# Kernel tuning notes

Measured on AMD Instinct MI355X. Metric: run time of the kernel, lower is better.

Reference implementation:

```python
import jax, jax.numpy as jnp
import numpy as np

N = 100000
E = 3200000
D = 64  # in_feats == hidden_feats == 64 (hardcoded in module)


def setup_inputs() -> dict:
    key = jax.random.key(0)
    ks = jax.random.split(key, 12)
    s = 1.0 / np.sqrt(D)
    return {
        "x": jax.random.normal(ks[0], (N, D), dtype=jnp.float32),
        "edge_index": jax.random.randint(ks[1], (2, E), 0, N, dtype=jnp.int64),
        "W1": jax.random.uniform(ks[2], (D, D), jnp.float32, -s, s),
        "b1": jnp.zeros((D,), jnp.float32),
        "W2": jax.random.uniform(ks[3], (D, D), jnp.float32, -s, s),
        "b2": jnp.zeros((D,), jnp.float32),
        "Wq": jax.random.uniform(ks[4], (D, D), jnp.float32, -s, s),
        "bq": jax.random.uniform(ks[5], (D,), jnp.float32, -s, s),
        "Wk": jax.random.uniform(ks[6], (D, D), jnp.float32, -s, s),
        "bk": jax.random.uniform(ks[7], (D,), jnp.float32, -s, s),
        "Wv": jax.random.uniform(ks[8], (D, D), jnp.float32, -s, s),
        "bv": jax.random.uniform(ks[9], (D,), jnp.float32, -s, s),
    }


def gcn_conv(x, src, dst, deg_inv_sqrt, W, b):
    # PyG GCNConv: linear -> normalized scatter-add over edges (self-loops included in src/dst)
    h = x @ W  # [N, D]
    norm = deg_inv_sqrt[src] * deg_inv_sqrt[dst]  # [E+N]
    msg = h[src] * norm[:, None]  # gather + scale
    out = jax.ops.segment_sum(msg, dst, num_segments=x.shape[0])  # scatter-add
    return out + b


def reference(x, edge_index, W1, b1, W2, b2, Wq, bq, Wk, bk, Wv, bv):
    n = x.shape[0]
    loop = jnp.arange(n, dtype=edge_index.dtype)
    src = jnp.concatenate([edge_index[0], loop])
    dst = jnp.concatenate([edge_index[1], loop])
    deg = jax.ops.segment_sum(jnp.ones_like(src, dtype=x.dtype), dst, num_segments=n)
    deg_inv_sqrt = jnp.where(deg > 0, jax.lax.rsqrt(deg), 0.0)

    h = jax.nn.relu(gcn_conv(x, src, dst, deg_inv_sqrt, W1, b1))
    # dropout with training=False -> identity; F.relu(relu(h)) == relu(h)
    h = jax.nn.relu(gcn_conv(h, src, dst, deg_inv_sqrt, W2, b2))

    # Attention with seq_len == 1
    q = h @ Wq + bq  # [N, D]
    k = h @ Wk + bk
    v = h @ Wv + bv
    scores = jnp.sum(q * k, axis=-1, keepdims=True)[:, :, None]  # [N,1,1]
    att = jax.nn.softmax(scores, axis=-1)  # == 1 for seq_len 1, kept for faithfulness
    context = att * v[:, None, :]  # [N,1,D]
    return context
```

## Files before the change

kernel.cpp:

```cpp
#include <hip/hip_runtime.h>
#include <hip/hip_bf16.h>
#include <cstdint>
#include <cstddef>


#define BN_SHIFT 8
#define BN 256
#define NBK 512
#define PCHUNK 4096
#define PCAP 16
#define BCAP 10240

static __device__ __forceinline__ uint32_t f32_to_bf16_bits(float f) {
    uint32_t u = __builtin_bit_cast(uint32_t, f);
    u += 0x7fffu + ((u >> 16) & 1u);
    return u >> 16;
}

static __device__ __forceinline__ void add_bf16x8(float* acc, uint4 q) {
    uint32_t w0 = q.x, w1 = q.y, w2 = q.z, w3 = q.w;
    acc[0] += __builtin_bit_cast(float, w0 << 16);
    acc[1] += __builtin_bit_cast(float, w0 & 0xffff0000u);
    acc[2] += __builtin_bit_cast(float, w1 << 16);
    acc[3] += __builtin_bit_cast(float, w1 & 0xffff0000u);
    acc[4] += __builtin_bit_cast(float, w2 << 16);
    acc[5] += __builtin_bit_cast(float, w2 & 0xffff0000u);
    acc[6] += __builtin_bit_cast(float, w3 << 16);
    acc[7] += __builtin_bit_cast(float, w3 & 0xffff0000u);
}

static __device__ __forceinline__ void scan_bcnt(const int* __restrict__ bcnt,
                                                 int* sbb, int* ssum) {
    int t = threadIdx.x;
    int c0 = bcnt[2 * t], c1 = bcnt[2 * t + 1];
    int v = c0 + c1;
    ssum[t] = v;
    __syncthreads();
    for (int o = 1; o < 256; o <<= 1) {
        int u = (t >= o) ? ssum[t - o] : 0;
        __syncthreads();
        ssum[t] += u;
        __syncthreads();
    }
    int ex = ssum[t] - v;
    sbb[2 * t] = ex;
    sbb[2 * t + 1] = ex + c0;
    if (t == 255) sbb[NBK] = ex + c0 + c1;
    __syncthreads();
}

__global__ __launch_bounds__(256) void hist_kernel(const int* __restrict__ ei,
                                                   int* __restrict__ pcnt, int E) {
    __shared__ int lc[NBK];
    int tid = threadIdx.x;
    lc[tid] = 0; lc[tid + 256] = 0;
    __syncthreads();

    int e0 = blockIdx.x * PCHUNK;
    int m = min(PCHUNK, E - e0);
    const int* dsts = ei + E + e0;
    if ((((uintptr_t)dsts) & 15) == 0) {
        int m4 = m >> 2;
        for (int t = tid; t < m4; t += 256) {
            int4 d = ((const int4*)dsts)[t];
            atomicAdd(&lc[d.x >> BN_SHIFT], 1);
            atomicAdd(&lc[d.y >> BN_SHIFT], 1);
            atomicAdd(&lc[d.z >> BN_SHIFT], 1);
            atomicAdd(&lc[d.w >> BN_SHIFT], 1);
        }
        for (int i = (m4 << 2) + tid; i < m; i += 256)
            atomicAdd(&lc[dsts[i] >> BN_SHIFT], 1);
    } else {
        for (int i = tid; i < m; i += 256)
            atomicAdd(&lc[dsts[i] >> BN_SHIFT], 1);
    }
    __syncthreads();
    int* row = pcnt + (size_t)blockIdx.x * NBK;
    row[tid] = lc[tid];
    row[tid + 256] = lc[tid + 256];
}

__global__ __launch_bounds__(256) void pscan_kernel(int* __restrict__ pcnt,
                                                    int* __restrict__ bcnt, int PB) {
    __shared__ int ss[256];
    int b = blockIdx.x;
    int tid = threadIdx.x;
    int iper = (PB + 255) >> 8;
    int i0 = tid * iper;
    int i1 = min(PB, i0 + iper);
    int vals[8];
    int s = 0;
    for (int i = i0, k = 0; i < i1; ++i, ++k) {
        vals[k] = pcnt[(size_t)i * NBK + b];
        s += vals[k];
    }
    ss[tid] = s;
    __syncthreads();
    for (int o = 1; o < 256; o <<= 1) {
        int u = (tid >= o) ? ss[tid - o] : 0;
        __syncthreads();
        ss[tid] += u;
        __syncthreads();
    }
    int run = ss[tid] - s;
    for (int i = i0, k = 0; i < i1; ++i, ++k) {
        pcnt[(size_t)i * NBK + b] = run;
        run += vals[k];
    }
    if (tid == 255) bcnt[b] = ss[255];
}

__global__ __launch_bounds__(256) void part_kernel(const int* __restrict__ ei,
                                                   const int* __restrict__ bcnt,
                                                   const int* __restrict__ poff,
                                                   uint32_t* __restrict__ stage, int E) {
    __shared__ int sbb[NBK + 1];
    __shared__ int ssum[256];
    __shared__ int cnt[NBK];
    __shared__ int base[NBK];
    __shared__ uint32_t bins[NBK * PCAP];
    int tid = threadIdx.x;
    scan_bcnt(bcnt, sbb, ssum);

    cnt[tid] = 0; cnt[tid + 256] = 0;
    {
        const int* prow = poff + (size_t)blockIdx.x * NBK;
        base[tid] = sbb[tid] + prow[tid];
        base[tid + 256] = sbb[tid + 256] + prow[tid + 256];
    }
    __syncthreads();

    int e0 = blockIdx.x * PCHUNK;
#pragma unroll
    for (int k = 0; k < PCHUNK / 256; ++k) {
        int e = e0 + (k << 8) + tid;
        if (e < E) {
            int s = ei[e];
            int d = ei[E + e];
            int b = d >> BN_SHIFT;
            uint32_t pack = (uint32_t)s | ((uint32_t)(d & (BN - 1)) << 17);
            int pos = atomicAdd(&cnt[b], 1);
            if (pos < PCAP) bins[b * PCAP + pos] = pack;
            else stage[base[b] + pos] = pack;
        }
    }
    __syncthreads();

    int wave = tid >> 6, lane = tid & 63;
    int sub = lane >> 4, idx = lane & 15;
    for (int b0 = wave * 4; b0 < NBK; b0 += 16) {
        int b = b0 + sub;
        int c = min(cnt[b], PCAP);
        if (idx < c) stage[base[b] + idx] = bins[b * PCAP + idx];
    }
}

__global__ __launch_bounds__(256) void build_kernel(const uint32_t* __restrict__ stage,
                                                    const int* __restrict__ bcnt,
                                                    int* __restrict__ rowptr,
                                                    float* __restrict__ dis,
                                                    int* __restrict__ col, int n) {
    __shared__ int sbb[NBK + 1];
    __shared__ uint32_t eb[BCAP];
    __shared__ int cnt[BN];
    __shared__ int off[BN];
    __shared__ int cur[BN];
    __shared__ int ssum[256];
    int tid = threadIdx.x;
    scan_bcnt(bcnt, sbb, ssum);
    int b = blockIdx.x;
    int node0 = b << BN_SHIFT;
    int ebase = sbb[b];
    int ecnt = sbb[b + 1] - ebase;
    int colbase = ebase + node0;

    cnt[tid] = 0;
    cur[tid] = 0;
    __syncthreads();

    bool fits = (ecnt <= BCAP);
    for (int i = tid; i < ecnt; i += 256) {
        uint32_t pk = stage[ebase + i];
        if (fits) eb[i] = pk;
        atomicAdd(&cnt[pk >> 17], 1);
    }
    __syncthreads();

    int c = cnt[tid] + 1;
    ssum[tid] = c;
    __syncthreads();
    for (int o = 1; o < 256; o <<= 1) {
        int u = (tid >= o) ? ssum[tid - o] : 0;
        __syncthreads();
        ssum[tid] += u;
        __syncthreads();
    }
    int ex = ssum[tid] - c;
    off[tid] = ex;
    int node = node0 + tid;
    if (node <= n) rowptr[node] = colbase + ex;
    if (node < n) {
        dis[node] = rsqrtf((float)c);
        col[colbase + ex] = node << 7;
    }
    __syncthreads();

    if (fits) {
        for (int i = tid; i < ecnt; i += 256) {
            uint32_t pk = eb[i];
            int doff = pk >> 17;
            int p = atomicAdd(&cur[doff], 1);
            col[colbase + off[doff] + 1 + p] = (int)(pk & 0x1ffff) << 7;
        }
    } else {
        for (int i = tid; i < ecnt; i += 256) {
            uint32_t pk = stage[ebase + i];
            int doff = pk >> 17;
            int p = atomicAdd(&cur[doff], 1);
            col[colbase + off[doff] + 1 + p] = (int)(pk & 0x1ffff) << 7;
        }
    }
}

template <int MODE>
__global__ __launch_bounds__(256) void gemm_kernel(const float* __restrict__ x,
                                                   const float* __restrict__ W,
                                                   const float* __restrict__ dis,
                                                   const float* __restrict__ bias,
                                                   void* __restrict__ out, int n) {
    __shared__ float Wl[64 * 64];
    int t = threadIdx.x;
    {
        const float4* W4 = (const float4*)W;
        float4* Wl4 = (float4*)Wl;
#pragma unroll
        for (int i = 0; i < 4; ++i) Wl4[t + i * 256] = W4[t + i * 256];
    }
    __syncthreads();

    int row = blockIdx.x * 256 + t;
    if (row >= n) return;

    const float4* xr = (const float4*)(x + (size_t)row * 64);
    float4 acc4[16];
#pragma unroll
    for (int p = 0; p < 16; ++p) acc4[p] = make_float4(0.f, 0.f, 0.f, 0.f);

    float4 xq = xr[0];
    for (int k4 = 0; k4 < 16; ++k4) {
        float4 xn = xq;
        if (k4 < 15) xn = xr[k4 + 1];
        float xs[4] = {xq.x, xq.y, xq.z, xq.w};
#pragma unroll
        for (int kk = 0; kk < 4; ++kk) {
            float xk = xs[kk];
            const float4* wr = (const float4*)&Wl[((k4 << 2) + kk) << 6];
#pragma unroll
            for (int j4 = 0; j4 < 16; ++j4) {
                float4 wv = wr[j4];
                acc4[j4].x = fmaf(xk, wv.x, acc4[j4].x);
                acc4[j4].y = fmaf(xk, wv.y, acc4[j4].y);
                acc4[j4].z = fmaf(xk, wv.z, acc4[j4].z);
                acc4[j4].w = fmaf(xk, wv.w, acc4[j4].w);
            }
        }
        xq = xn;
    }

    if (MODE == 0) {
        float s = dis[row];
        uint4* go = (uint4*)out;
#pragma unroll
        for (int p = 0; p < 8; ++p) {
            float4 a = acc4[2 * p];
            float4 bq = acc4[2 * p + 1];
            uint4 o;
            o.x = (f32_to_bf16_bits(a.y * s) << 16) | f32_to_bf16_bits(a.x * s);
            o.y = (f32_to_bf16_bits(a.w * s) << 16) | f32_to_bf16_bits(a.z * s);
            o.z = (f32_to_bf16_bits(bq.y * s) << 16) | f32_to_bf16_bits(bq.x * s);
            o.w = (f32_to_bf16_bits(bq.w * s) << 16) | f32_to_bf16_bits(bq.z * s);
            go[(size_t)row * 8 + p] = o;
        }
    } else {
        const float4* b4 = (const float4*)bias;
        float4* fo = (float4*)out;
#pragma unroll
        for (int p = 0; p < 16; ++p) {
            float4 bb = b4[p];
            float4 a = acc4[p];
            a.x += bb.x; a.y += bb.y; a.z += bb.z; a.w += bb.w;
            fo[(size_t)row * 16 + p] = a;
        }
    }
}

__global__ __launch_bounds__(256) void agg_kernel(const char* __restrict__ g,
                                                  const int* __restrict__ rowptr,
                                                  const int* __restrict__ col,
                                                  const float* __restrict__ dis,
                                                  const float* __restrict__ bias,
                                                  float* __restrict__ out, int n) {
    int tid = threadIdx.x;
    int wave = tid >> 6, lane = tid & 63;
    int grp = lane >> 3, chk = lane & 7;
    int node = blockIdx.x * 32 + (wave << 3) + grp;
    if (node >= n) return;

    const char* gc = g + (chk << 4);

    float acc[8];
#pragma unroll
    for (int j = 0; j < 8; ++j) acc[j] = 0.f;

    int e = rowptr[node];
    int end = rowptr[node + 1];
    for (; e + 1 < end; e += 2) {
        int o0 = col[e];
        int o1 = col[e + 1];
        uint4 q0 = *(const uint4*)(gc + o0);
        uint4 q1 = *(const uint4*)(gc + o1);
        add_bf16x8(acc, q0);
        add_bf16x8(acc, q1);
    }
    if (e < end) add_bf16x8(acc, *(const uint4*)(gc + col[e]));

    float dv = dis[node];
    const float4* b4 = (const float4*)bias;
    float4 bb0 = b4[chk * 2], bb1 = b4[chk * 2 + 1];
    float4 o0, o1;
    o0.x = fmaxf(fmaf(acc[0], dv, bb0.x), 0.f);
    o0.y = fmaxf(fmaf(acc[1], dv, bb0.y), 0.f);
    o0.z = fmaxf(fmaf(acc[2], dv, bb0.z), 0.f);
    o0.w = fmaxf(fmaf(acc[3], dv, bb0.w), 0.f);
    o1.x = fmaxf(fmaf(acc[4], dv, bb1.x), 0.f);
    o1.y = fmaxf(fmaf(acc[5], dv, bb1.y), 0.f);
    o1.z = fmaxf(fmaf(acc[6], dv, bb1.z), 0.f);
    o1.w = fmaxf(fmaf(acc[7], dv, bb1.w), 0.f);
    float4* fo = (float4*)(out + (size_t)node * 64 + (chk << 3));
    fo[0] = o0;
    fo[1] = o1;
}

extern "C" void kernel_launch(void* const* d_in, const int* in_sizes, int n_in,
                              void* d_out, int out_size, void* d_ws, size_t ws_size,
                              hipStream_t stream) {
    const float* x  = (const float*)d_in[0];
    const int*   ei = (const int*)d_in[1];
    const float* W1 = (const float*)d_in[2];
    const float* b1 = (const float*)d_in[3];
    const float* W2 = (const float*)d_in[4];
    const float* b2 = (const float*)d_in[5];
    const float* Wv = (const float*)d_in[10];
    const float* bv = (const float*)d_in[11];

    const int N = in_sizes[0] / 64;
    const int E = in_sizes[1] / 2;
    const int NB = (N + BN - 1) >> BN_SHIFT;
    const int PB = (E + PCHUNK - 1) / PCHUNK;

    auto align_up = [](size_t v) { return (v + 255) & ~(size_t)255; };
    char* p = (char*)d_ws;
    int*   rowptr = (int*)p;    p += align_up((size_t)(N + 1) * 4);
    float* dis    = (float*)p;  p += align_up((size_t)N * 4);
    int*   pcnt   = (int*)p;    p += align_up((size_t)PB * NBK * 4);
    int*   bcnt   = (int*)p;    p += align_up((size_t)NBK * 4);
    int*   col    = (int*)p;    p += align_up((size_t)(E + N + BN) * 4);
    size_t gsz    = (size_t)N * 128 > (size_t)E * 4 ? (size_t)N * 128 : (size_t)E * 4;
    char*  gbuf   = p;          p += align_up(gsz);
    float* xbuf   = (float*)p;  p += align_up((size_t)N * 256);
    uint32_t* stage = (uint32_t*)gbuf;

    int nbl = (N + 255) / 256;
    int abl = (N + 31) / 32;

    hist_kernel <<<PB, 256, 0, stream>>>(ei, pcnt, E);
    pscan_kernel<<<NBK, 256, 0, stream>>>(pcnt, bcnt, PB);
    part_kernel <<<PB, 256, 0, stream>>>(ei, bcnt, pcnt, stage, E);
    build_kernel<<<NB, 256, 0, stream>>>(stage, bcnt, rowptr, dis, col, N);

    gemm_kernel<0><<<nbl, 256, 0, stream>>>(x, W1, dis, nullptr, gbuf, N);
    agg_kernel<<<abl, 256, 0, stream>>>(gbuf, rowptr, col, dis, b1, xbuf, N);

    gemm_kernel<0><<<nbl, 256, 0, stream>>>(xbuf, W2, dis, nullptr, gbuf, N);
    agg_kernel<<<abl, 256, 0, stream>>>(gbuf, rowptr, col, dis, b2, xbuf, N);

    gemm_kernel<1><<<nbl, 256, 0, stream>>>(xbuf, Wv, nullptr, bv, d_out, N);
}
```

Measured before the change: 367.2 us.

## Split bf16 feature table into four column panels and aggregate per panel

The GEMM now writes the scaled bf16 features as four 32-byte panels of 16 columns each, stored panel-major, instead of one 128-byte row per node. Aggregation launches a 2D grid over the panels. Each wave handles one node at a time: 8 lane groups take interleaved edges, each lane gathers a 4-byte pair of features, and the partial sums are combined with xor shuffles. The intent is that each panel (about 3.2 MB) stays resident in cache during the random gathers, and that edge-level parallelism balances high-degree nodes. In exchange, every col index is read four times, each gather is only 4 bytes, the shuffles add cost, and each node's work per wave is serialized.

```diff
diff --git a/kernel.cpp b/kernel.cpp
--- a/kernel.cpp
+++ b/kernel.cpp
@@ -17,16 +17,8 @@
     return u >> 16;
 }
 
-static __device__ __forceinline__ void add_bf16x8(float* acc, uint4 q) {
-    uint32_t w0 = q.x, w1 = q.y, w2 = q.z, w3 = q.w;
-    acc[0] += __builtin_bit_cast(float, w0 << 16);
-    acc[1] += __builtin_bit_cast(float, w0 & 0xffff0000u);
-    acc[2] += __builtin_bit_cast(float, w1 << 16);
-    acc[3] += __builtin_bit_cast(float, w1 & 0xffff0000u);
-    acc[4] += __builtin_bit_cast(float, w2 << 16);
-    acc[5] += __builtin_bit_cast(float, w2 & 0xffff0000u);
-    acc[6] += __builtin_bit_cast(float, w3 << 16);
-    acc[7] += __builtin_bit_cast(float, w3 & 0xffff0000u);
+static __device__ __forceinline__ float bfhi(uint32_t w) {
+    return __builtin_bit_cast(float, w);
 }
 
 static __device__ __forceinline__ void scan_bcnt(const int* __restrict__ bcnt,
@@ -201,7 +193,7 @@
     if (node <= n) rowptr[node] = colbase + ex;
     if (node < n) {
         dis[node] = rsqrtf((float)c);
-        col[colbase + ex] = node << 7;
+        col[colbase + ex] = node << 5;
     }
     __syncthreads();
 
@@ -210,14 +202,14 @@
             uint32_t pk = eb[i];
             int doff = pk >> 17;
             int p = atomicAdd(&cur[doff], 1);
-            col[colbase + off[doff] + 1 + p] = (int)(pk & 0x1ffff) << 7;
+            col[colbase + off[doff] + 1 + p] = (int)(pk & 0x1ffff) << 5;
         }
     } else {
         for (int i = tid; i < ecnt; i += 256) {
             uint32_t pk = stage[ebase + i];
             int doff = pk >> 17;
             int p = atomicAdd(&cur[doff], 1);
-            col[colbase + off[doff] + 1 + p] = (int)(pk & 0x1ffff) << 7;
+            col[colbase + off[doff] + 1 + p] = (int)(pk & 0x1ffff) << 5;
         }
     }
 }
@@ -269,17 +261,24 @@
 
     if (MODE == 0) {
         float s = dis[row];
-        uint4* go = (uint4*)out;
-#pragma unroll
-        for (int p = 0; p < 8; ++p) {
-            float4 a = acc4[2 * p];
-            float4 bq = acc4[2 * p + 1];
-            uint4 o;
-            o.x = (f32_to_bf16_bits(a.y * s) << 16) | f32_to_bf16_bits(a.x * s);
-            o.y = (f32_to_bf16_bits(a.w * s) << 16) | f32_to_bf16_bits(a.z * s);
-            o.z = (f32_to_bf16_bits(bq.y * s) << 16) | f32_to_bf16_bits(bq.x * s);
-            o.w = (f32_to_bf16_bits(bq.w * s) << 16) | f32_to_bf16_bits(bq.z * s);
-            go[(size_t)row * 8 + p] = o;
+        char* gp = (char*)out;
+        size_t pstr = (size_t)n * 32;
+#pragma unroll
+        for (int q = 0; q < 4; ++q) {
+            float4 a0 = acc4[4 * q + 0], a1 = acc4[4 * q + 1];
+            float4 a2 = acc4[4 * q + 2], a3 = acc4[4 * q + 3];
+            uint4 o0, o1;
+            o0.x = (f32_to_bf16_bits(a0.y * s) << 16) | f32_to_bf16_bits(a0.x * s);
+            o0.y = (f32_to_bf16_bits(a0.w * s) << 16) | f32_to_bf16_bits(a0.z * s);
+            o0.z = (f32_to_bf16_bits(a1.y * s) << 16) | f32_to_bf16_bits(a1.x * s);
+            o0.w = (f32_to_bf16_bits(a1.w * s) << 16) | f32_to_bf16_bits(a1.z * s);
+            o1.x = (f32_to_bf16_bits(a2.y * s) << 16) | f32_to_bf16_bits(a2.x * s);
+            o1.y = (f32_to_bf16_bits(a2.w * s) << 16) | f32_to_bf16_bits(a2.z * s);
+            o1.z = (f32_to_bf16_bits(a3.y * s) << 16) | f32_to_bf16_bits(a3.x * s);
+            o1.w = (f32_to_bf16_bits(a3.w * s) << 16) | f32_to_bf16_bits(a3.z * s);
+            uint4* dst = (uint4*)(gp + q * pstr + (size_t)row * 32);
+            dst[0] = o0;
+            dst[1] = o1;
         }
     } else {
         const float4* b4 = (const float4*)bias;
@@ -299,46 +298,51 @@
                                                   const int* __restrict__ col,
                                                   const float* __restrict__ dis,
                                                   const float* __restrict__ bias,
-                                                  float* __restrict__ out, int n) {
+                                                  float* __restrict__ out,
+                                                  int n, int pstr) {
     int tid = threadIdx.x;
     int wave = tid >> 6, lane = tid & 63;
     int grp = lane >> 3, chk = lane & 7;
-    int node = blockIdx.x * 32 + (wave << 3) + grp;
-    if (node >= n) return;
-
-    const char* gc = g + (chk << 4);
-
-    float acc[8];
-#pragma unroll
-    for (int j = 0; j < 8; ++j) acc[j] = 0.f;
-
-    int e = rowptr[node];
-    int end = rowptr[node + 1];
-    for (; e + 1 < end; e += 2) {
-        int o0 = col[e];
-        int o1 = col[e + 1];
-        uint4 q0 = *(const uint4*)(gc + o0);
-        uint4 q1 = *(const uint4*)(gc + o1);
-        add_bf16x8(acc, q0);
-        add_bf16x8(acc, q1);
-    }
-    if (e < end) add_bf16x8(acc, *(const uint4*)(gc + col[e]));
-
-    float dv = dis[node];
-    const float4* b4 = (const float4*)bias;
-    float4 bb0 = b4[chk * 2], bb1 = b4[chk * 2 + 1];
-    float4 o0, o1;
-    o0.x = fmaxf(fmaf(acc[0], dv, bb0.x), 0.f);
-    o0.y = fmaxf(fmaf(acc[1], dv, bb0.y), 0.f);
-    o0.z = fmaxf(fmaf(acc[2], dv, bb0.z), 0.f);
-    o0.w = fmaxf(fmaf(acc[3], dv, bb0.w), 0.f);
-    o1.x = fmaxf(fmaf(acc[4], dv, bb1.x), 0.f);
-    o1.y = fmaxf(fmaf(acc[5], dv, bb1.y), 0.f);
-    o1.z = fmaxf(fmaf(acc[6], dv, bb1.z), 0.f);
-    o1.w = fmaxf(fmaf(acc[7], dv, bb1.w), 0.f);
-    float4* fo = (float4*)(out + (size_t)node * 64 + (chk << 3));
-    fo[0] = o0;
-    fo[1] = o1;
+    int q = blockIdx.y;
+    const char* gp = g + (size_t)q * pstr + (chk << 2);
+    int f = (q << 4) + (chk << 1);
+    float b0 = bias[f], b1 = bias[f + 1];
+
+    int nbase = blockIdx.x * 16 + wave * 4;
+#pragma unroll
+    for (int t = 0; t < 4; ++t) {
+        int node = nbase + t;
+        if (node >= n) return;
+
+        float ax = 0.f, ay = 0.f;
+        int beg = rowptr[node];
+        int end = rowptr[node + 1];
+        int e = beg + grp;
+        for (; e + 8 < end; e += 16) {
+            uint32_t w0 = *(const uint32_t*)(gp + col[e]);
+            uint32_t w1 = *(const uint32_t*)(gp + col[e + 8]);
+            ax += bfhi(w0 << 16); ay += bfhi(w0 & 0xffff0000u);
+            ax += bfhi(w1 << 16); ay += bfhi(w1 & 0xffff0000u);
+        }
+        if (e < end) {
+            uint32_t w = *(const uint32_t*)(gp + col[e]);
+            ax += bfhi(w << 16); ay += bfhi(w & 0xffff0000u);
+        }
+
+#pragma unroll
+        for (int m = 8; m < 64; m <<= 1) {
+            ax += __shfl_xor(ax, m, 64);
+            ay += __shfl_xor(ay, m, 64);
+        }
+
+        if (grp == 0) {
+            float dv = dis[node];
+            float2 o;
+            o.x = fmaxf(fmaf(ax, dv, b0), 0.f);
+            o.y = fmaxf(fmaf(ay, dv, b1), 0.f);
+            *(float2*)(out + (size_t)node * 64 + f) = o;
+        }
+    }
 }
 
 extern "C" void kernel_launch(void* const* d_in, const int* in_sizes, int n_in,
@@ -371,7 +375,8 @@
     uint32_t* stage = (uint32_t*)gbuf;
 
     int nbl = (N + 255) / 256;
-    int abl = (N + 31) / 32;
+    dim3 agrid((N + 15) / 16, 4);
+    int pstr = N * 32;
 
     hist_kernel <<<PB, 256, 0, stream>>>(ei, pcnt, E);
     pscan_kernel<<<NBK, 256, 0, stream>>>(pcnt, bcnt, PB);
@@ -379,10 +384,10 @@
     build_kernel<<<NB, 256, 0, stream>>>(stage, bcnt, rowptr, dis, col, N);
 
     gemm_kernel<0><<<nbl, 256, 0, stream>>>(x, W1, dis, nullptr, gbuf, N);
-    agg_kernel<<<abl, 256, 0, stream>>>(gbuf, rowptr, col, dis, b1, xbuf, N);
+    agg_kernel<<<agrid, 256, 0, stream>>>(gbuf, rowptr, col, dis, b1, xbuf, N, pstr);
 
     gemm_kernel<0><<<nbl, 256, 0, stream>>>(xbuf, W2, dis, nullptr, gbuf, N);
-    agg_kernel<<<abl, 256, 0, stream>>>(gbuf, rowptr, col, dis, b2, xbuf, N);
+    agg_kernel<<<agrid, 256, 0, stream>>>(gbuf, rowptr, col, dis, b2, xbuf, N, pstr);
 
     gemm_kernel<1><<<nbl, 256, 0, stream>>>(xbuf, Wv, nullptr, bv, d_out, N);
 }
```

Result: slower. 512.7 us (+39.6%).

## Assign one wavefront per node in aggregation and drop LDS edge buffer in build

Applied to the files above, without the earlier changes.

The aggregation kernel now gives each node a full 64-lane wavefront instead of 8 lanes. Eight lane groups stride over the node's edges with a 4-way unrolled gather, and partial sums are combined with xor shuffles before one group writes the output. This is meant to expose more memory-level parallelism per node for the irregular gather, at the cost of idle lanes on low-degree nodes and extra shuffle work. The build kernel also drops its 40 KB shared-memory edge cache and rereads the stage buffer from global memory, which lowers LDS use and should raise occupancy but adds a second global read.

```diff
diff --git a/kernel.cpp b/kernel.cpp
--- a/kernel.cpp
+++ b/kernel.cpp
@@ -9,7 +9,6 @@
 #define NBK 512
 #define PCHUNK 4096
 #define PCAP 16
-#define BCAP 10240
 
 static __device__ __forceinline__ uint32_t f32_to_bf16_bits(float f) {
     uint32_t u = __builtin_bit_cast(uint32_t, f);
@@ -161,11 +160,10 @@
                                                     float* __restrict__ dis,
                                                     int* __restrict__ col, int n) {
     __shared__ int sbb[NBK + 1];
-    __shared__ uint32_t eb[BCAP];
+    __shared__ int ssum[256];
     __shared__ int cnt[BN];
     __shared__ int off[BN];
     __shared__ int cur[BN];
-    __shared__ int ssum[256];
     int tid = threadIdx.x;
     scan_bcnt(bcnt, sbb, ssum);
     int b = blockIdx.x;
@@ -178,12 +176,8 @@
     cur[tid] = 0;
     __syncthreads();
 
-    bool fits = (ecnt <= BCAP);
-    for (int i = tid; i < ecnt; i += 256) {
-        uint32_t pk = stage[ebase + i];
-        if (fits) eb[i] = pk;
-        atomicAdd(&cnt[pk >> 17], 1);
-    }
+    for (int i = tid; i < ecnt; i += 256)
+        atomicAdd(&cnt[stage[ebase + i] >> 17], 1);
     __syncthreads();
 
     int c = cnt[tid] + 1;
@@ -205,20 +199,11 @@
     }
     __syncthreads();
 
-    if (fits) {
-        for (int i = tid; i < ecnt; i += 256) {
-            uint32_t pk = eb[i];
-            int doff = pk >> 17;
-            int p = atomicAdd(&cur[doff], 1);
-            col[colbase + off[doff] + 1 + p] = (int)(pk & 0x1ffff) << 7;
-        }
-    } else {
-        for (int i = tid; i < ecnt; i += 256) {
-            uint32_t pk = stage[ebase + i];
-            int doff = pk >> 17;
-            int p = atomicAdd(&cur[doff], 1);
-            col[colbase + off[doff] + 1 + p] = (int)(pk & 0x1ffff) << 7;
-        }
+    for (int i = tid; i < ecnt; i += 256) {
+        uint32_t pk = stage[ebase + i];
+        int doff = pk >> 17;
+        int p = atomicAdd(&cur[doff], 1);
+        col[colbase + off[doff] + 1 + p] = (int)(pk & 0x1ffff) << 7;
     }
 }
 
@@ -300,45 +285,59 @@
                                                   const float* __restrict__ dis,
                                                   const float* __restrict__ bias,
                                                   float* __restrict__ out, int n) {
-    int tid = threadIdx.x;
-    int wave = tid >> 6, lane = tid & 63;
-    int grp = lane >> 3, chk = lane & 7;
-    int node = blockIdx.x * 32 + (wave << 3) + grp;
-    if (node >= n) return;
-
-    const char* gc = g + (chk << 4);
+    int wid = (blockIdx.x * 256 + threadIdx.x) >> 6;
+    if (wid >= n) return;
+    int lane = threadIdx.x & 63;
+    int grp = lane >> 3;
+    int chk16 = (lane & 7) << 4;
+    const char* gc = g + chk16;
 
     float acc[8];
 #pragma unroll
     for (int j = 0; j < 8; ++j) acc[j] = 0.f;
 
-    int e = rowptr[node];
-    int end = rowptr[node + 1];
-    for (; e + 1 < end; e += 2) {
+    int e = rowptr[wid] + grp;
+    int end = rowptr[wid + 1];
+    for (; e + 24 < end; e += 32) {
         int o0 = col[e];
-        int o1 = col[e + 1];
+        int o1 = col[e + 8];
+        int o2 = col[e + 16];
+        int o3 = col[e + 24];
         uint4 q0 = *(const uint4*)(gc + o0);
         uint4 q1 = *(const uint4*)(gc + o1);
+        uint4 q2 = *(const uint4*)(gc + o2);
+        uint4 q3 = *(const uint4*)(gc + o3);
         add_bf16x8(acc, q0);
         add_bf16x8(acc, q1);
-    }
-    if (e < end) add_bf16x8(acc, *(const uint4*)(gc + col[e]));
-
-    float dv = dis[node];
-    const float4* b4 = (const float4*)bias;
-    float4 bb0 = b4[chk * 2], bb1 = b4[chk * 2 + 1];
-    float4 o0, o1;
-    o0.x = fmaxf(fmaf(acc[0], dv, bb0.x), 0.f);
-    o0.y = fmaxf(fmaf(acc[1], dv, bb0.y), 0.f);
-    o0.z = fmaxf(fmaf(acc[2], dv, bb0.z), 0.f);
-    o0.w = fmaxf(fmaf(acc[3], dv, bb0.w), 0.f);
-    o1.x = fmaxf(fmaf(acc[4], dv, bb1.x), 0.f);
-    o1.y = fmaxf(fmaf(acc[5], dv, bb1.y), 0.f);
-    o1.z = fmaxf(fmaf(acc[6], dv, bb1.z), 0.f);
-    o1.w = fmaxf(fmaf(acc[7], dv, bb1.w), 0.f);
-    float4* fo = (float4*)(out + (size_t)node * 64 + (chk << 3));
-    fo[0] = o0;
-    fo[1] = o1;
+        add_bf16x8(acc, q2);
+        add_bf16x8(acc, q3);
+    }
+    for (; e < end; e += 8) {
+        add_bf16x8(acc, *(const uint4*)(gc + col[e]));
+    }
+
+#pragma unroll
+    for (int m = 8; m < 64; m <<= 1) {
+#pragma unroll
+        for (int j = 0; j < 8; ++j) acc[j] += __shfl_xor(acc[j], m, 64);
+    }
+
+    if (grp == 0) {
+        float dv = dis[wid];
+        float4 o0, o1;
+        const float* bb = bias + (chk16 >> 1);
+        o0.x = fmaxf(fmaf(acc[0], dv, bb[0]), 0.f);
+        o0.y = fmaxf(fmaf(acc[1], dv, bb[1]), 0.f);
+        o0.z = fmaxf(fmaf(acc[2], dv, bb[2]), 0.f);
+        o0.w = fmaxf(fmaf(acc[3], dv, bb[3]), 0.f);
+        o1.x = fmaxf(fmaf(acc[4], dv, bb[4]), 0.f);
+        o1.y = fmaxf(fmaf(acc[5], dv, bb[5]), 0.f);
+        o1.z = fmaxf(fmaf(acc[6], dv, bb[6]), 0.f);
+        o1.w = fmaxf(fmaf(acc[7], dv, bb[7]), 0.f);
+        float4* fo = (float4*)out;
+        fo[(size_t)wid * 16 + (chk16 >> 3) + 0] = o0;
+        fo[(size_t)wid * 16 + (chk16 >> 3) + 1] = o1;
+    }
 }
 
 extern "C" void kernel_launch(void* const* d_in, const int* in_sizes, int n_in,
@@ -371,7 +370,7 @@
     uint32_t* stage = (uint32_t*)gbuf;
 
     int nbl = (N + 255) / 256;
-    int abl = (N + 31) / 32;
+    int abl = (N + 3) / 4;
 
     hist_kernel <<<PB, 256, 0, stream>>>(ei, pcnt, E);
     pscan_kernel<<<NBK, 256, 0, stream>>>(pcnt, bcnt, PB);
```

New measurement: 362.9 us. About the same (-1.2%).
